# Kernel tuning notes

Hardware: AMD Instinct MI355X
Metric: run time of the kernel (lower is better)

Reference implementation:

```python
import jax, jax.numpy as jnp
import numpy as np

LAMB = 1.0
EPS = 1e-16


def setup_inputs() -> dict:
    key = jax.random.key(0)
    kx, km = jax.random.split(key)
    N, D, K = 262144, 128, 64
    x = jax.random.normal(kx, (N, D), dtype=jnp.float32)
    m = jax.random.normal(km, (K, D), dtype=jnp.float32)
    m = m / jnp.linalg.norm(m, axis=1, keepdims=True)  # unit-norm rows like __init__
    return {"x": x, "m": m}


def _entropy(p):
    # replicate torch.where clamping
    p = jnp.where(p <= 0, EPS, p)
    p = jnp.where(p >= 1, 1.0 - EPS, p)
    return -jnp.sum(p * jnp.log(p), axis=-1)


def _p(x, m):
    d2 = (jnp.sum(x * x, axis=-1, keepdims=True)
          - 2.0 * x @ m.T
          + jnp.sum(m * m, axis=-1))  # [N, K]
    return jax.nn.softmax(-d2, axis=-1)


def reference(x, m):
    p = _p(x, m)                      # [N, K]
    intra = jnp.mean(_entropy(p))     # scalar
    mu = jnp.mean(m, axis=0)          # [D]
    p_inter = _p(mu[None, :], m)[0]   # [K]
    inter = _entropy(p_inter)
    total = intra - LAMB * inter
    return (total, intra, inter)
```

## Files before the change

kernel.cpp:

```cpp
#include <hip/hip_runtime.h>

#define D 128
#define K 64

typedef __attribute__((ext_vector_type(8))) short short8;
typedef __attribute__((ext_vector_type(2))) int int2v;
typedef __attribute__((ext_vector_type(4))) float f32x4;

__device__ inline short f2bf(float f) {
  union { float f; unsigned u; } v; v.f = f;
  unsigned u = v.u;
  return (short)((u + 0x7fffu + ((u >> 16) & 1u)) >> 16);
}

__device__ inline int cvt_pk_bf16(float lo, float hi) {
  int r;
  asm("v_cvt_pk_bf16_f32 %0, %1, %2" : "=v"(r) : "v"(lo), "v"(hi));
  return r;
}

template<int CTRL>
__device__ inline float dpp_ror(float x) {
  return __builtin_bit_cast(float, __builtin_amdgcn_update_dpp(
      0, __builtin_bit_cast(int, x), CTRL, 0xF, 0xF, true));
}
__device__ inline float rowsum16(float v) {
  v += dpp_ror<0x121>(v);
  v += dpp_ror<0x122>(v);
  v += dpp_ror<0x124>(v);
  v += dpp_ror<0x128>(v);
  return v;
}
__device__ inline float rowmax16(float v) {
  v = fmaxf(v, dpp_ror<0x121>(v));
  v = fmaxf(v, dpp_ror<0x122>(v));
  v = fmaxf(v, dpp_ror<0x124>(v));
  v = fmaxf(v, dpp_ror<0x128>(v));
  return v;
}

#define LOADX(dst, t) do {                                                  \
    const f32x4* xb = (const f32x4*)(x + (size_t)(t) * (16 * D)) + lane;    \
    _Pragma("unroll") for (int p = 0; p < 8; ++p) dst[p] = xb[p * 64];      \
  } while (0)

#define PACKX(src) do {                                                     \
    _Pragma("unroll") for (int p = 0; p < 8; ++p) {                         \
      f32x4 v = src[p];                                                     \
      int2v s;                                                              \
      s[0] = cvt_pk_bf16(v[0], v[1]);                                       \
      s[1] = cvt_pk_bf16(v[2], v[3]);                                       \
      int r = 2 * p + hi;                                                   \
      *(int2v*)(amem + r * 256 + ((wc ^ r) << 4) + wh * 8) = s;             \
    }                                                                       \
  } while (0)

#define TILE_COMPUTE() do {                                                 \
    f32x4 acc[4];                                                           \
    _Pragma("unroll") for (int jt = 0; jt < 4; ++jt)                        \
      acc[jt] = (f32x4){0.f, 0.f, 0.f, 0.f};                                \
    _Pragma("unroll") for (int kk = 0; kk < 4; ++kk) {                      \
      short8 afrag = *(const short8*)(amem + ra[kk]);                       \
      _Pragma("unroll") for (int jt = 0; jt < 4; ++jt)                      \
        acc[jt] = __builtin_amdgcn_mfma_f32_16x16x32_bf16(                  \
            afrag, bsm[cbase[kk] + jt * 256], acc[jt], 0, 0, 0);            \
    }                                                                       \
    _Pragma("unroll") for (int r = 0; r < 4; ++r) {                         \
      float s0 = acc[0][r] - mn[0];                                         \
      float s1 = acc[1][r] - mn[1];                                         \
      float s2 = acc[2][r] - mn[2];                                         \
      float s3 = acc[3][r] - mn[3];                                         \
      float mx = rowmax16(fmaxf(fmaxf(s0, s1), fmaxf(s2, s3)));             \
      float t0 = s0 - mx, t1 = s1 - mx, t2 = s2 - mx, t3 = s3 - mx;         \
      float e0 = __expf(t0), e1 = __expf(t1);                               \
      float e2 = __expf(t2), e3 = __expf(t3);                               \
      float S0 = rowsum16((e0 + e1) + (e2 + e3));                           \
      float S1 = rowsum16((t0 * e0 + t1 * e1) + (t2 * e2 + t3 * e3));       \
      float H = __logf(S0) - S1 / S0;                                       \
      hacc += (lid == 0) ? H : 0.0f;                                        \
    }                                                                       \
  } while (0)

__launch_bounds__(256, 4)
__global__ void main_kernel(const float* __restrict__ x, const float* __restrict__ m,
                            float* ws, int nTiles, int totalWaves) {
  __shared__ short8 bsm[1024];
  __shared__ float mnorms[K];
  __shared__ char asmem[4][4096];

  const int tid = threadIdx.x;
  for (int i = tid; i < K * D; i += 256) {
    int c = i >> 3, e = i & 7;
    int cs = c ^ ((c >> 4) & 7);
    ((short*)bsm)[cs * 8 + e] = f2bf(2.0f * m[i]);
  }
  if (tid < K) {
    const float* mr = m + tid * D;
    float s = 0.f;
    for (int d = 0; d < D; ++d) s += mr[d] * mr[d];
    mnorms[tid] = s;
  }
  __syncthreads();

  const int lane = tid & 63;
  const int lid  = lane & 15;
  const int quad = lane >> 4;
  const int wid  = tid >> 6;
  char* amem = asmem[wid];

  float mn[4];
#pragma unroll
  for (int jt = 0; jt < 4; ++jt) mn[jt] = mnorms[jt * 16 + lid];

  int cbase[4], ra[4];
#pragma unroll
  for (int kk = 0; kk < 4; ++kk) {
    cbase[kk] = (lid * 16 + kk * 4 + quad) ^ (lid & 7);
    ra[kk] = lid * 256 + ((((kk << 2) | quad) ^ lid) << 4);
  }

  const int hi = lane >> 5;
  const int wc = (lane & 31) >> 1;
  const int wh = lane & 1;

  const int wave = blockIdx.x * 4 + wid;
  const int step = 2 * totalWaves;
  float hacc = 0.f;

  f32x4 ldA[8], ldB[8];
  int tA = wave, tB = wave + totalWaves;
  const int iters = nTiles / step;
  if (tA < nTiles) LOADX(ldA, tA);
  if (tB < nTiles) LOADX(ldB, tB);

  for (int it = 0; it < iters; ++it) {
    const bool more = (it + 1 < iters);
    PACKX(ldA);
    if (more) LOADX(ldA, tA + step);
    TILE_COMPUTE();
    PACKX(ldB);
    if (more) LOADX(ldB, tB + step);
    TILE_COMPUTE();
    tA += step; tB += step;
  }
  for (int t = wave + iters * step; t < nTiles; t += totalWaves) {
    LOADX(ldA, t);
    PACKX(ldA);
    TILE_COMPUTE();
  }

  for (int off = 1; off < 64; off <<= 1) hacc += __shfl_xor(hacc, off, 64);
  __shared__ float red[4];
  if (lane == 0) red[wid] = hacc;
  __syncthreads();
  if (tid == 0) atomicAdd(ws, red[0] + red[1] + red[2] + red[3]);
}

__global__ void final_kernel(const float* __restrict__ m, const float* ws, float* out, int nRows) {
  __shared__ float mu[D];
  int lane = threadIdx.x;
  for (int d = lane; d < D; d += 64) {
    float s = 0.f;
    for (int j = 0; j < K; ++j) s += m[j * D + d];
    mu[d] = s * (1.0f / K);
  }
  __syncthreads();
  const float* mr = m + lane * D;
  float dot = 0.f, nrm = 0.f;
  for (int d = 0; d < D; ++d) {
    dot += mu[d] * mr[d];
    nrm += mr[d] * mr[d];
  }
  float s = 2.f * dot - nrm;
  float mx = s;
  for (int off = 1; off < 64; off <<= 1) mx = fmaxf(mx, __shfl_xor(mx, off, 64));
  float t = s - mx;
  float e = __expf(t);
  float S0 = e, S1 = t * e;
  for (int off = 1; off < 64; off <<= 1) {
    S0 += __shfl_xor(S0, off, 64);
    S1 += __shfl_xor(S1, off, 64);
  }
  float inter = __logf(S0) - S1 / S0;
  if (lane == 0) {
    float intra = ws[0] / (float)nRows;
    out[0] = intra - inter;
    out[1] = intra;
    out[2] = inter;
  }
}

extern "C" void kernel_launch(void* const* d_in, const int* in_sizes, int n_in,
                              void* d_out, int out_size, void* d_ws, size_t ws_size,
                              hipStream_t stream) {
  const float* x = (const float*)d_in[0];
  const float* m = (const float*)d_in[1];
  float* ws = (float*)d_ws;
  float* out = (float*)d_out;
  const int N = in_sizes[0] / D;
  const int nTiles = N / 16;

  hipMemsetAsync(ws, 0, 64, stream);

  const int blocks = 1024;
  const int totalWaves = blocks * 4;
  main_kernel<<<blocks, 256, 0, stream>>>(x, m, ws, nTiles, totalWaves);

  final_kernel<<<1, 64, 0, stream>>>(m, ws, out, N);
}
```

Measured before the change: 204.8 us.

## Issue all four tile loads upfront and replace atomic with per-block partials

Each wave now loads at most four 16-row tiles into registers at the start, then packs and computes them in sequence, replacing the double-buffered loop. The launch bound drops to 2 blocks per SM so the extra registers fit. The global atomicAdd and the memset are replaced by per-block partial sums that the final kernel reduces. This assumes nTiles is at most 4*totalWaves; larger inputs would silently skip rows, and lower occupancy may hurt latency hiding.

```diff
diff --git a/kernel.cpp b/kernel.cpp
--- a/kernel.cpp
+++ b/kernel.cpp
@@ -81,7 +81,7 @@
     }                                                                       \
   } while (0)
 
-__launch_bounds__(256, 4)
+__launch_bounds__(256, 2)
 __global__ void main_kernel(const float* __restrict__ x, const float* __restrict__ m,
                             float* ws, int nTiles, int totalWaves) {
   __shared__ short8 bsm[1024];
@@ -124,39 +124,32 @@
   const int wh = lane & 1;
 
   const int wave = blockIdx.x * 4 + wid;
-  const int step = 2 * totalWaves;
   float hacc = 0.f;
 
-  f32x4 ldA[8], ldB[8];
-  int tA = wave, tB = wave + totalWaves;
-  const int iters = nTiles / step;
-  if (tA < nTiles) LOADX(ldA, tA);
-  if (tB < nTiles) LOADX(ldB, tB);
-
-  for (int it = 0; it < iters; ++it) {
-    const bool more = (it + 1 < iters);
-    PACKX(ldA);
-    if (more) LOADX(ldA, tA + step);
-    TILE_COMPUTE();
-    PACKX(ldB);
-    if (more) LOADX(ldB, tB + step);
-    TILE_COMPUTE();
-    tA += step; tB += step;
-  }
-  for (int t = wave + iters * step; t < nTiles; t += totalWaves) {
-    LOADX(ldA, t);
-    PACKX(ldA);
-    TILE_COMPUTE();
-  }
+  f32x4 ld0[8], ld1[8], ld2[8], ld3[8];
+  const int t0 = wave;
+  const int t1 = wave + totalWaves;
+  const int t2 = wave + 2 * totalWaves;
+  const int t3 = wave + 3 * totalWaves;
+  LOADX(ld0, t0);
+  if (t1 < nTiles) LOADX(ld1, t1);
+  if (t2 < nTiles) LOADX(ld2, t2);
+  if (t3 < nTiles) LOADX(ld3, t3);
+
+  PACKX(ld0); TILE_COMPUTE();
+  if (t1 < nTiles) { PACKX(ld1); TILE_COMPUTE(); }
+  if (t2 < nTiles) { PACKX(ld2); TILE_COMPUTE(); }
+  if (t3 < nTiles) { PACKX(ld3); TILE_COMPUTE(); }
 
   for (int off = 1; off < 64; off <<= 1) hacc += __shfl_xor(hacc, off, 64);
   __shared__ float red[4];
   if (lane == 0) red[wid] = hacc;
   __syncthreads();
-  if (tid == 0) atomicAdd(ws, red[0] + red[1] + red[2] + red[3]);
-}
-
-__global__ void final_kernel(const float* __restrict__ m, const float* ws, float* out, int nRows) {
+  if (tid == 0) ws[blockIdx.x] = red[0] + red[1] + red[2] + red[3];
+}
+
+__global__ void final_kernel(const float* __restrict__ m, const float* ws, float* out,
+                             int nRows, int nBlocks) {
   __shared__ float mu[D];
   int lane = threadIdx.x;
   for (int d = lane; d < D; d += 64) {
@@ -165,6 +158,11 @@
     mu[d] = s * (1.0f / K);
   }
   __syncthreads();
+
+  float part = 0.f;
+  for (int i = lane; i < nBlocks; i += 64) part += ws[i];
+  for (int off = 1; off < 64; off <<= 1) part += __shfl_xor(part, off, 64);
+
   const float* mr = m + lane * D;
   float dot = 0.f, nrm = 0.f;
   for (int d = 0; d < D; ++d) {
@@ -183,7 +181,7 @@
   }
   float inter = __logf(S0) - S1 / S0;
   if (lane == 0) {
-    float intra = ws[0] / (float)nRows;
+    float intra = part / (float)nRows;
     out[0] = intra - inter;
     out[1] = intra;
     out[2] = inter;
@@ -200,11 +198,9 @@
   const int N = in_sizes[0] / D;
   const int nTiles = N / 16;
 
-  hipMemsetAsync(ws, 0, 64, stream);
-
   const int blocks = 1024;
   const int totalWaves = blocks * 4;
   main_kernel<<<blocks, 256, 0, stream>>>(x, m, ws, nTiles, totalWaves);
 
-  final_kernel<<<1, 64, 0, stream>>>(m, ws, out, N);
-}
+  final_kernel<<<1, 64, 0, stream>>>(m, ws, out, N, blocks);
+}
```

Result: no change. 201.8 us (-1.5%).
